# Performance work log

Hardware: AMD Instinct MI355X
Metric: run time of the kernel (lower is better)

## Reference

```python
import jax, jax.numpy as jnp
import numpy as np

K = 20
HID = 64
NUM_CLASSES = 50
BIG = 1e10  # effectively-infinite distance for self-loop exclusion


def knn_idx(x, k):
    # x: [N, d] -> idx: [N, k] indices of k nearest neighbors in feature space (excluding self)
    sq = jnp.sum(x * x, axis=1)
    dist = sq[:, None] + sq[None, :] - 2.0 * (x @ x.T)  # [N, N]
    n = x.shape[0]
    dist = dist.at[jnp.arange(n), jnp.arange(n)].set(BIG)
    _, idx = jax.lax.top_k(-dist, k)
    return idx


def edge_conv(x, k, W, b):
    # DynamicEdgeConv: message = relu(Linear(cat[x_i, x_j - x_i])), aggr = max over k neighbors
    idx = knn_idx(x, k)                      # [N, k]
    xj = x[idx]                              # [N, k, d] neighbor gather
    xi = jnp.broadcast_to(x[:, None, :], xj.shape)
    feat = jnp.concatenate([xi, xj - xi], axis=-1)   # [N, k, 2d]
    h = jax.nn.relu(jnp.einsum('nkf,fo->nko', feat, W) + b)
    return jnp.max(h, axis=1)                # [N, out]


def setup_inputs() -> dict:
    key = jax.random.key(0)
    ks = jax.random.split(key, 16)
    def lin(kw, fan_in, fan_out):
        s = 1.0 / np.sqrt(fan_in)
        return jax.random.uniform(kw, (fan_in, fan_out), jnp.float32, -s, s)
    inp = {
        'x':  jax.random.normal(ks[0], (8192, 3), jnp.float32),
        'W1': lin(ks[1], 2 * 3, HID),      'b1': jnp.zeros((HID,), jnp.float32),
        'W2': lin(ks[2], 2 * HID, HID),    'b2': jnp.zeros((HID,), jnp.float32),
        'W3': lin(ks[3], 2 * HID, HID),    'b3': jnp.zeros((HID,), jnp.float32),
        'Wl': lin(ks[4], 3 * HID, 1024),   'bl': jnp.zeros((1024,), jnp.float32),
        'Wm1': lin(ks[5], 1024, 256),      'bm1': jnp.zeros((256,), jnp.float32),
        'Wm2': lin(ks[6], 256, 128),       'bm2': jnp.zeros((128,), jnp.float32),
        'Wo': lin(ks[7], 128, NUM_CLASSES),'bo': jnp.zeros((NUM_CLASSES,), jnp.float32),
    }
    return inp


def reference(x, W1, b1, W2, b2, W3, b3, Wl, bl, Wm1, bm1, Wm2, bm2, Wo, bo):
    x1 = edge_conv(x, K, W1, b1)     # [N, 64], kNN on raw 3-D points
    x2 = edge_conv(x1, K, W2, b2)    # [N, 64], kNN recomputed in feature space
    x3 = edge_conv(x2, K, W3, b3)    # [N, 64]
    h = jnp.concatenate([x1, x2, x3], axis=1)            # [N, 192]
    h = jax.nn.relu(h @ Wl + bl)                         # lin1: MLP([192, 1024])
    h = jax.nn.relu(h @ Wm1 + bm1)                       # MLP([1024, 256]) (dropout: eval mode)
    h = jax.nn.relu(h @ Wm2 + bm2)                       # MLP([256, 128])
    out = h @ Wo + bo                                    # final Linear
    return jax.nn.log_softmax(out, axis=-1)
```

## Files before the change

### kernel.cpp

```cpp
#include <hip/hip_runtime.h>
#include <math.h>

#define NPTS 8192
#define KNN 20
#define NLISTS 32

#define OFF_SQ   0
#define OFF_IDX  8192
#define OFF_A    172032
#define OFF_B    696320
#define OFF_CAT  1220608
#define OFF_H1   2793472
#define OFF_H2   11182080
#define OFF_H3   13279232
#define OFF_PART OFF_H1
#define OFF_PACK (OFF_H1 + 5242880)
#define PACK_ELEMS 262144
#define OFF_WT   OFF_A

typedef __attribute__((ext_vector_type(8))) short bf16x8;
typedef __attribute__((ext_vector_type(16))) float f32x16;

__device__ inline unsigned umed3(unsigned a, unsigned b, unsigned c) {
    unsigned d;
    asm("v_med3_u32 %0, %1, %2, %3" : "=v"(d) : "v"(a), "v"(b), "v"(c));
    return d;
}

__device__ inline unsigned short f2bf(float f) {
    unsigned u = __float_as_uint(f);
    u += 0x7FFFu + ((u >> 16) & 1u);
    return (unsigned short)(u >> 16);
}

template<int D>
__global__ __launch_bounds__(256)
void sqnorm_kernel(const float* __restrict__ X, int stride, float* __restrict__ sq) {
    int n = blockIdx.x * blockDim.x + threadIdx.x;
    if (n < NPTS) {
        float s = 0.f;
        #pragma unroll
        for (int f = 0; f < D; ++f) {
            float v = X[(size_t)n * stride + f];
            s = fmaf(v, v, s);
        }
        sq[n] = s;
    }
}

template<int D, int KP>
__global__ __launch_bounds__(256)
void prepack_kernel(const float* __restrict__ X, int stride,
                    unsigned short* __restrict__ Xhi, unsigned short* __restrict__ Xlo,
                    unsigned short* __restrict__ Yhi, unsigned short* __restrict__ Ylo) {
    int t2 = blockIdx.x * 256 + threadIdx.x;
    int t = t2 * 2;
    int n = t >> (KP == 64 ? 6 : 4);
    int k = t & (KP - 1);
    float xv[2];
    xv[0] = (k     < D) ? X[(size_t)n * stride + k]     : 0.f;
    xv[1] = (k + 1 < D) ? X[(size_t)n * stride + k + 1] : 0.f;
    ushort2 hx, lx, hy, ly;
    unsigned short* hxp = (unsigned short*)&hx;
    unsigned short* lxp = (unsigned short*)&lx;
    unsigned short* hyp = (unsigned short*)&hy;
    unsigned short* lyp = (unsigned short*)&ly;
    #pragma unroll
    for (int e = 0; e < 2; ++e) {
        float x = xv[e];
        unsigned short hi = f2bf(x);
        float hif = __uint_as_float((unsigned)hi << 16);
        unsigned short lo = f2bf(x - hif);
        float y = -2.f * x;
        unsigned short yhi = f2bf(y);
        float yhif = __uint_as_float((unsigned)yhi << 16);
        unsigned short ylo = f2bf(y - yhif);
        hxp[e] = hi; lxp[e] = lo; hyp[e] = yhi; lyp[e] = ylo;
    }
    *(ushort2*)&Xhi[t] = hx;
    *(ushort2*)&Xlo[t] = lx;
    *(ushort2*)&Yhi[t] = hy;
    *(ushort2*)&Ylo[t] = ly;
}

template<int K, int NBITS>
__global__ __launch_bounds__(256)
void prepack_w(const float* __restrict__ W,
               unsigned short* __restrict__ Thi, unsigned short* __restrict__ Tlo) {
    const int N = 1 << NBITS;
    int t = blockIdx.x * 256 + threadIdx.x;
    int k = t >> NBITS, n = t & (N - 1);
    float x = W[t];
    unsigned short hi = f2bf(x);
    float hif = __uint_as_float((unsigned)hi << 16);
    unsigned short lo = f2bf(x - hif);
    Thi[(size_t)n * K + k] = hi;
    Tlo[(size_t)n * K + k] = lo;
}

template<int KP>
__global__ __launch_bounds__(256, 4)
void knnA_mfma(const unsigned short* __restrict__ Yhi, const unsigned short* __restrict__ Ylo,
               const unsigned short* __restrict__ Xhi, const unsigned short* __restrict__ Xlo,
               const float* __restrict__ sq, unsigned int* __restrict__ part) {
    constexpr int NS = KP / 16;
    constexpr int NT = 8;
    const int wave = threadIdx.x >> 6, lane = threadIdx.x & 63;
    const int col = lane & 31;
    const int h   = lane >> 5;
    const int bi  = (blockIdx.x * 4 + wave) * 32 + col;
    const int jbase = blockIdx.y * 256;

    bf16x8 bhi[NS], blo[NS];
    #pragma unroll
    for (int s = 0; s < NS; ++s) {
        bhi[s] = *(const bf16x8*)&Xhi[(size_t)bi * KP + s * 16 + h * 8];
        blo[s] = *(const bf16x8*)&Xlo[(size_t)bi * KP + s * 16 + h * 8];
    }
    const float sqi = sq[bi];

    unsigned top[KNN];
    #pragma unroll
    for (int k = 0; k < KNN; ++k) top[k] = 0xFFFFFFFFu;

    for (int jt = 0; jt < NT; ++jt) {
        const int j0 = jbase + jt * 32;
        const int aj = j0 + col;
        f32x16 C;
        #pragma unroll
        for (int q = 0; q < 4; ++q) {
            const float4 s4 = *(const float4*)&sq[j0 + h * 4 + q * 8];
            C[q * 4 + 0] = sqi + s4.x;
            C[q * 4 + 1] = sqi + s4.y;
            C[q * 4 + 2] = sqi + s4.z;
            C[q * 4 + 3] = sqi + s4.w;
        }
        #pragma unroll
        for (int s = 0; s < NS; ++s) {
            bf16x8 ahi = *(const bf16x8*)&Yhi[(size_t)aj * KP + s * 16 + h * 8];
            bf16x8 alo = *(const bf16x8*)&Ylo[(size_t)aj * KP + s * 16 + h * 8];
            C = __builtin_amdgcn_mfma_f32_32x32x16_bf16(ahi, bhi[s], C, 0, 0, 0);
            C = __builtin_amdgcn_mfma_f32_32x32x16_bf16(ahi, blo[s], C, 0, 0, 0);
            C = __builtin_amdgcn_mfma_f32_32x32x16_bf16(alo, bhi[s], C, 0, 0, 0);
        }
        #pragma unroll
        for (int q = 0; q < 4; ++q) {
            const int jq = j0 + h * 4 + q * 8;
            #pragma unroll
            for (int t = 0; t < 4; ++t) {
                const int j = jq + t;
                float d = fmaxf(C[q * 4 + t], 0.f);
                unsigned key = (__float_as_uint(d) & 0xFFFFE000u) | (unsigned)j;
                if (j == bi) key = 0xFFFFFFFFu;
                #pragma unroll
                for (int p = KNN - 1; p >= 1; --p)
                    top[p] = umed3(key, top[p - 1], top[p]);
                top[0] = min(top[0], key);
            }
        }
    }

    {
        bool done = false;
        #pragma unroll
        for (int k = 0; k < KNN; ++k) {
            unsigned c = __shfl_xor(top[k], 32);
            if (!done) done = __all(c >= top[KNN - 1]);
            if (!done) {
                #pragma unroll
                for (int p = KNN - 1; p >= 1; --p)
                    top[p] = umed3(c, top[p - 1], top[p]);
                top[0] = min(top[0], c);
            }
        }
    }

    if (h == 0) {
        unsigned* o = part + ((size_t)bi * NLISTS + blockIdx.y) * KNN;
        #pragma unroll
        for (int k = 0; k < KNN; ++k) o[k] = top[k];
    }
}

__global__ __launch_bounds__(256)
void knnB_kernel(const unsigned int* __restrict__ part, int* __restrict__ idx_out) {
    const int wave = threadIdx.x >> 6, lane = threadIdx.x & 63;
    const int half = lane >> 5;
    const int l = lane & 31;
    const int row = (blockIdx.x * 4 + wave) * 2 + half;

    unsigned top[KNN];
    const unsigned* p = part + ((size_t)row * NLISTS + l) * KNN;
    #pragma unroll
    for (int k = 0; k < KNN; k += 4) {
        uint4 v = *(const uint4*)(p + k);
        top[k] = v.x; top[k + 1] = v.y; top[k + 2] = v.z; top[k + 3] = v.w;
    }

    #pragma unroll
    for (int mi = 0; mi < 5; ++mi) {
        const int m = 1 << mi;
        bool done = false;
        #pragma unroll
        for (int k = 0; k < KNN; ++k) {
            unsigned c = __shfl_xor(top[k], m);
            if (!done) done = __all(c >= top[KNN - 1]);
            if (!done) {
                #pragma unroll
                for (int q = KNN - 1; q >= 1; --q)
                    top[q] = umed3(c, top[q - 1], top[q]);
                top[0] = min(top[0], c);
            }
        }
    }

    if (l == 0) {
        #pragma unroll
        for (int k = 0; k < KNN; ++k)
            idx_out[(size_t)row * KNN + k] = (int)(top[k] & 0x1FFFu);
    }
}

template<int D>
__global__ __launch_bounds__(256)
void featAB_kernel(const float* __restrict__ X, int stride, const float* __restrict__ W,
                   float* __restrict__ A, float* __restrict__ B) {
    const int wave = threadIdx.x >> 6, lane = threadIdx.x & 63;
    const int n = blockIdx.x * 4 + wave;
    float a = 0.f, b = 0.f;
    const float* xp = X + (size_t)n * stride;
    #pragma unroll
    for (int f = 0; f < D; ++f) {
        float xf = xp[f];
        a = fmaf(xf, W[(size_t)f * 64 + lane], a);
        b = fmaf(xf, W[(size_t)(D + f) * 64 + lane], b);
    }
    A[(size_t)n * 64 + lane] = a;
    B[(size_t)n * 64 + lane] = b;
}

__global__ __launch_bounds__(256)
void edge_fuse_kernel(const float* __restrict__ A, const float* __restrict__ B,
                      const int* __restrict__ idx, const float* __restrict__ bias,
                      float* __restrict__ out, int ostride,
                      float* __restrict__ sqo,
                      unsigned short* __restrict__ Xhi, unsigned short* __restrict__ Xlo,
                      unsigned short* __restrict__ Yhi, unsigned short* __restrict__ Ylo) {
    const int wave = threadIdx.x >> 6, lane = threadIdx.x & 63;
    const int n = blockIdx.x * 4 + wave;
    const float base = A[(size_t)n * 64 + lane] - B[(size_t)n * 64 + lane] + bias[lane];
    float m = -INFINITY;
    #pragma unroll 4
    for (int k = 0; k < KNN; ++k) {
        int j = idx[(size_t)n * KNN + k];
        m = fmaxf(m, base + B[(size_t)j * 64 + lane]);
    }
    m = fmaxf(m, 0.f);
    out[(size_t)n * ostride + lane] = m;

    float s = m * m;
    #pragma unroll
    for (int off = 32; off; off >>= 1) s += __shfl_xor(s, off);
    if (lane == 0) sqo[n] = s;

    unsigned short hi = f2bf(m);
    float hif = __uint_as_float((unsigned)hi << 16);
    unsigned short lo = f2bf(m - hif);
    float y = -2.f * m;
    unsigned short yhi = f2bf(y);
    float yhif = __uint_as_float((unsigned)yhi << 16);
    unsigned short ylo = f2bf(y - yhif);
    Xhi[(size_t)n * 64 + lane] = hi;
    Xlo[(size_t)n * 64 + lane] = lo;
    Yhi[(size_t)n * 64 + lane] = yhi;
    Ylo[(size_t)n * 64 + lane] = ylo;
}

__global__ __launch_bounds__(256)
void edge_agg_kernel(const float* __restrict__ A, const float* __restrict__ B,
                     const int* __restrict__ idx, const float* __restrict__ bias,
                     float* __restrict__ out, int ostride) {
    const int wave = threadIdx.x >> 6, lane = threadIdx.x & 63;
    const int n = blockIdx.x * 4 + wave;
    const float base = A[(size_t)n * 64 + lane] - B[(size_t)n * 64 + lane] + bias[lane];
    float m = -INFINITY;
    #pragma unroll 4
    for (int k = 0; k < KNN; ++k) {
        int j = idx[(size_t)n * KNN + k];
        m = fmaxf(m, base + B[(size_t)j * 64 + lane]);
    }
    out[(size_t)n * ostride + lane] = fmaxf(m, 0.f);
}

template<int K, int N, int CTW>
__global__ __launch_bounds__(256, 3)
void gemm_mfma_relu(const float* __restrict__ A,
                    const unsigned short* __restrict__ Whi, const unsigned short* __restrict__ Wlo,
                    const float* __restrict__ bias, float* __restrict__ C) {
    const int wave = threadIdx.x >> 6, lane = threadIdx.x & 63;
    const int col = lane & 31, h = lane >> 5;
    const int r0 = blockIdx.x * 32;
    const int nb = blockIdx.y * (CTW * 128) + wave * (CTW * 32);
    const float* arow = A + (size_t)(r0 + col) * K + h * 8;

    f32x16 acc[CTW];
    #pragma unroll
    for (int c = 0; c < CTW; ++c)
        #pragma unroll
        for (int r = 0; r < 16; ++r) acc[c][r] = 0.f;

    #pragma unroll 4
    for (int s = 0; s < K / 16; ++s) {
        float4 f0 = *(const float4*)(arow + s * 16);
        float4 f1 = *(const float4*)(arow + s * 16 + 4);
        bf16x8 ahi, alo;
        {
            float xv[8] = {f0.x, f0.y, f0.z, f0.w, f1.x, f1.y, f1.z, f1.w};
            #pragma unroll
            for (int e = 0; e < 8; ++e) {
                unsigned u = __float_as_uint(xv[e]);
                ahi[e] = (short)(u >> 16);
                float d = xv[e] - __uint_as_float(u & 0xFFFF0000u);
                alo[e] = (short)(__float_as_uint(d) >> 16);
            }
        }
        #pragma unroll
        for (int c = 0; c < CTW; ++c) {
            const size_t wb = (size_t)(nb + c * 32 + col) * K + s * 16 + h * 8;
            bf16x8 bhi = *(const bf16x8*)&Whi[wb];
            bf16x8 blo = *(const bf16x8*)&Wlo[wb];
            acc[c] = __builtin_amdgcn_mfma_f32_32x32x16_bf16(ahi, bhi, acc[c], 0, 0, 0);
            acc[c] = __builtin_amdgcn_mfma_f32_32x32x16_bf16(alo, bhi, acc[c], 0, 0, 0);
            acc[c] = __builtin_amdgcn_mfma_f32_32x32x16_bf16(ahi, blo, acc[c], 0, 0, 0);
        }
    }

    #pragma unroll
    for (int c = 0; c < CTW; ++c) {
        const int n = nb + c * 32 + col;
        const float b = bias[n];
        #pragma unroll
        for (int q = 0; q < 4; ++q)
            #pragma unroll
            for (int t = 0; t < 4; ++t) {
                const int rl = 4 * h + 8 * q + t;
                C[(size_t)(r0 + rl) * N + n] = fmaxf(acc[c][q * 4 + t] + b, 0.f);
            }
    }
}

__global__ __launch_bounds__(256)
void final_kernel(const float* __restrict__ H, const float* __restrict__ Wo,
                  const float* __restrict__ bo, float* __restrict__ out) {
    const int wave = threadIdx.x >> 6, lane = threadIdx.x & 63;
    const int n = blockIdx.x * 4 + wave;
    float v = -INFINITY;
    if (lane < 50) {
        float a = bo[lane];
        const float* h = H + (size_t)n * 128;
        #pragma unroll 4
        for (int f = 0; f < 128; ++f) a = fmaf(h[f], Wo[f * 50 + lane], a);
        v = a;
    }
    float mx = v;
    #pragma unroll
    for (int off = 32; off; off >>= 1) mx = fmaxf(mx, __shfl_xor(mx, off));
    float e = (lane < 50) ? expf(v - mx) : 0.f;
    float s = e;
    #pragma unroll
    for (int off = 32; off; off >>= 1) s += __shfl_xor(s, off);
    if (lane < 50) out[(size_t)n * 50 + lane] = v - mx - logf(s);
}

extern "C" void kernel_launch(void* const* d_in, const int* in_sizes, int n_in,
                              void* d_out, int out_size, void* d_ws, size_t ws_size,
                              hipStream_t stream) {
    const float* x   = (const float*)d_in[0];
    const float* W1  = (const float*)d_in[1];
    const float* b1  = (const float*)d_in[2];
    const float* W2  = (const float*)d_in[3];
    const float* b2  = (const float*)d_in[4];
    const float* W3  = (const float*)d_in[5];
    const float* b3  = (const float*)d_in[6];
    const float* Wl  = (const float*)d_in[7];
    const float* bl  = (const float*)d_in[8];
    const float* Wm1 = (const float*)d_in[9];
    const float* bm1 = (const float*)d_in[10];
    const float* Wm2 = (const float*)d_in[11];
    const float* bm2 = (const float*)d_in[12];
    const float* Wo  = (const float*)d_in[13];
    const float* bo  = (const float*)d_in[14];

    float* ws   = (float*)d_ws;
    float* sq   = ws + OFF_SQ;
    int*   idx  = (int*)(ws + OFF_IDX);
    float* Abuf = ws + OFF_A;
    float* Bbuf = ws + OFF_B;
    float* cat  = ws + OFF_CAT;
    float* h1   = ws + OFF_H1;
    unsigned int* part = (unsigned int*)(ws + OFF_PART);
    unsigned short* Phi = (unsigned short*)(ws + OFF_PACK);
    unsigned short* Plo = (unsigned short*)(ws + OFF_PACK + PACK_ELEMS);
    unsigned short* Qhi = (unsigned short*)(ws + OFF_PACK + 2 * PACK_ELEMS);
    unsigned short* Qlo = (unsigned short*)(ws + OFF_PACK + 3 * PACK_ELEMS);
    float* h2   = ws + OFF_H2;
    float* h3   = ws + OFF_H3;
    unsigned short* WlT_hi  = (unsigned short*)(ws + OFF_WT);
    unsigned short* WlT_lo  = (unsigned short*)(ws + OFF_WT + 98304);
    unsigned short* Wm1T_hi = (unsigned short*)(ws + OFF_WT + 196608);
    unsigned short* Wm1T_lo = (unsigned short*)(ws + OFF_WT + 327680);
    unsigned short* Wm2T_hi = (unsigned short*)(ws + OFF_WT + 458752);
    unsigned short* Wm2T_lo = (unsigned short*)(ws + OFF_WT + 475136);
    float* out  = (float*)d_out;

    dim3 b256(256);
    dim3 gknn(64, 32);

    sqnorm_kernel<3><<<32, b256, 0, stream>>>(x, 3, sq);
    prepack_kernel<3, 16><<<256, b256, 0, stream>>>(x, 3, Phi, Plo, Qhi, Qlo);
    knnA_mfma<16><<<gknn, b256, 0, stream>>>(Qhi, Qlo, Phi, Plo, sq, part);
    knnB_kernel<<<1024, b256, 0, stream>>>(part, idx);
    featAB_kernel<3><<<2048, b256, 0, stream>>>(x, 3, W1, Abuf, Bbuf);
    edge_fuse_kernel<<<2048, b256, 0, stream>>>(Abuf, Bbuf, idx, b1, cat + 0, 192,
                                                sq, Phi, Plo, Qhi, Qlo);

    knnA_mfma<64><<<gknn, b256, 0, stream>>>(Qhi, Qlo, Phi, Plo, sq, part);
    knnB_kernel<<<1024, b256, 0, stream>>>(part, idx);
    featAB_kernel<64><<<2048, b256, 0, stream>>>(cat + 0, 192, W2, Abuf, Bbuf);
    edge_fuse_kernel<<<2048, b256, 0, stream>>>(Abuf, Bbuf, idx, b2, cat + 64, 192,
                                                sq, Phi, Plo, Qhi, Qlo);

    knnA_mfma<64><<<gknn, b256, 0, stream>>>(Qhi, Qlo, Phi, Plo, sq, part);
    knnB_kernel<<<1024, b256, 0, stream>>>(part, idx);
    featAB_kernel<64><<<2048, b256, 0, stream>>>(cat + 64, 192, W3, Abuf, Bbuf);
    edge_agg_kernel<<<2048, b256, 0, stream>>>(Abuf, Bbuf, idx, b3, cat + 128, 192);

    prepack_w<192, 10><<<768, b256, 0, stream>>>(Wl, WlT_hi, WlT_lo);
    prepack_w<1024, 8><<<1024, b256, 0, stream>>>(Wm1, Wm1T_hi, Wm1T_lo);
    prepack_w<256, 7><<<128, b256, 0, stream>>>(Wm2, Wm2T_hi, Wm2T_lo);

    dim3 g1(256, 4);
    gemm_mfma_relu<192, 1024, 2><<<g1, b256, 0, stream>>>(cat, WlT_hi, WlT_lo, bl, h1);
    dim3 g2(256, 1);
    gemm_mfma_relu<1024, 256, 2><<<g2, b256, 0, stream>>>(h1, Wm1T_hi, Wm1T_lo, bm1, h2);
    dim3 g3(256, 1);
    gemm_mfma_relu<256, 128, 1><<<g3, b256, 0, stream>>>(h2, Wm2T_hi, Wm2T_lo, bm2, h3);
    final_kernel<<<2048, b256, 0, stream>>>(h3, Wo, bo, out);
}
```

Measured before the change: 523.0 us.

## Software-pipeline kNN MFMA tiles with double-buffered accumulators and prefetched operands

Restructures the kNN distance loop in knnA_mfma to process two 32-column tiles per iteration with two accumulators, so the top-k insertion of one tile can overlap the MFMA chain of the next. Operand fragments for the next tiles are loaded ahead of use. The launch bound drops from 4 to 2 blocks per SM to give room for the extra registers. Lower occupancy may reduce latency hiding elsewhere.

```diff
diff --git a/kernel.cpp b/kernel.cpp
--- a/kernel.cpp
+++ b/kernel.cpp
@@ -98,8 +98,26 @@
     Tlo[(size_t)n * K + k] = lo;
 }
 
+#define PROCESS(Cv, j0base)                                                    \
+    do {                                                                       \
+        _Pragma("unroll")                                                      \
+        for (int q = 0; q < 4; ++q) {                                          \
+            _Pragma("unroll")                                                  \
+            for (int t = 0; t < 4; ++t) {                                      \
+                const int j = (j0base) + h * 4 + q * 8 + t;                    \
+                float dd = fmaxf((Cv)[q * 4 + t], 0.f);                        \
+                unsigned key = (__float_as_uint(dd) & 0xFFFFE000u) | (unsigned)j; \
+                if (j == bi) key = 0xFFFFFFFFu;                                \
+                _Pragma("unroll")                                              \
+                for (int p = KNN - 1; p >= 1; --p)                             \
+                    top[p] = umed3(key, top[p - 1], top[p]);                   \
+                top[0] = min(top[0], key);                                     \
+            }                                                                  \
+        }                                                                      \
+    } while (0)
+
 template<int KP>
-__global__ __launch_bounds__(256, 4)
+__global__ __launch_bounds__(256, 2)
 void knnA_mfma(const unsigned short* __restrict__ Yhi, const unsigned short* __restrict__ Ylo,
                const unsigned short* __restrict__ Xhi, const unsigned short* __restrict__ Xlo,
                const float* __restrict__ sq, unsigned int* __restrict__ part) {
@@ -123,42 +141,72 @@
     #pragma unroll
     for (int k = 0; k < KNN; ++k) top[k] = 0xFFFFFFFFu;
 
-    for (int jt = 0; jt < NT; ++jt) {
-        const int j0 = jbase + jt * 32;
+    bf16x8 fA[NS], fB[NS], lo[NS];
+    f32x16 CCa, CCb;
+
+    {
+        const size_t a0 = (size_t)(jbase + col) * KP + h * 8;
+        #pragma unroll
+        for (int s = 0; s < NS; ++s)
+            fA[s] = *(const bf16x8*)&Yhi[a0 + s * 16];
+    }
+
+    #pragma unroll 1
+    for (int jt2 = 0; jt2 < NT; jt2 += 2) {
+        const int j0 = jbase + jt2 * 32;
         const int aj = j0 + col;
-        f32x16 C;
-        #pragma unroll
-        for (int q = 0; q < 4; ++q) {
-            const float4 s4 = *(const float4*)&sq[j0 + h * 4 + q * 8];
-            C[q * 4 + 0] = sqi + s4.x;
-            C[q * 4 + 1] = sqi + s4.y;
-            C[q * 4 + 2] = sqi + s4.z;
-            C[q * 4 + 3] = sqi + s4.w;
-        }
+
+        #pragma unroll
+        for (int s = 0; s < NS; ++s)
+            fB[s] = *(const bf16x8*)&Yhi[(size_t)(aj + 32) * KP + s * 16 + h * 8];
+        #pragma unroll
+        for (int s = 0; s < NS; ++s)
+            lo[s] = *(const bf16x8*)&Ylo[(size_t)aj * KP + s * 16 + h * 8];
+        float4 e0 = *(const float4*)&sq[j0 + h * 4];
+        float4 e1 = *(const float4*)&sq[j0 + h * 4 + 8];
+        float4 e2 = *(const float4*)&sq[j0 + h * 4 + 16];
+        float4 e3 = *(const float4*)&sq[j0 + h * 4 + 24];
+
+        if (jt2 > 0) PROCESS(CCb, j0 - 32);
+
+        CCa[0] = sqi + e0.x; CCa[1] = sqi + e0.y; CCa[2]  = sqi + e0.z; CCa[3]  = sqi + e0.w;
+        CCa[4] = sqi + e1.x; CCa[5] = sqi + e1.y; CCa[6]  = sqi + e1.z; CCa[7]  = sqi + e1.w;
+        CCa[8] = sqi + e2.x; CCa[9] = sqi + e2.y; CCa[10] = sqi + e2.z; CCa[11] = sqi + e2.w;
+        CCa[12] = sqi + e3.x; CCa[13] = sqi + e3.y; CCa[14] = sqi + e3.z; CCa[15] = sqi + e3.w;
         #pragma unroll
         for (int s = 0; s < NS; ++s) {
-            bf16x8 ahi = *(const bf16x8*)&Yhi[(size_t)aj * KP + s * 16 + h * 8];
-            bf16x8 alo = *(const bf16x8*)&Ylo[(size_t)aj * KP + s * 16 + h * 8];
-            C = __builtin_amdgcn_mfma_f32_32x32x16_bf16(ahi, bhi[s], C, 0, 0, 0);
-            C = __builtin_amdgcn_mfma_f32_32x32x16_bf16(ahi, blo[s], C, 0, 0, 0);
-            C = __builtin_amdgcn_mfma_f32_32x32x16_bf16(alo, bhi[s], C, 0, 0, 0);
-        }
-        #pragma unroll
-        for (int q = 0; q < 4; ++q) {
-            const int jq = j0 + h * 4 + q * 8;
+            CCa = __builtin_amdgcn_mfma_f32_32x32x16_bf16(fA[s], bhi[s], CCa, 0, 0, 0);
+            CCa = __builtin_amdgcn_mfma_f32_32x32x16_bf16(fA[s], blo[s], CCa, 0, 0, 0);
+            CCa = __builtin_amdgcn_mfma_f32_32x32x16_bf16(lo[s], bhi[s], CCa, 0, 0, 0);
+        }
+
+        if (jt2 + 2 < NT) {
             #pragma unroll
-            for (int t = 0; t < 4; ++t) {
-                const int j = jq + t;
-                float d = fmaxf(C[q * 4 + t], 0.f);
-                unsigned key = (__float_as_uint(d) & 0xFFFFE000u) | (unsigned)j;
-                if (j == bi) key = 0xFFFFFFFFu;
-                #pragma unroll
-                for (int p = KNN - 1; p >= 1; --p)
-                    top[p] = umed3(key, top[p - 1], top[p]);
-                top[0] = min(top[0], key);
-            }
-        }
-    }
+            for (int s = 0; s < NS; ++s)
+                fA[s] = *(const bf16x8*)&Yhi[(size_t)(aj + 64) * KP + s * 16 + h * 8];
+        }
+        #pragma unroll
+        for (int s = 0; s < NS; ++s)
+            lo[s] = *(const bf16x8*)&Ylo[(size_t)(aj + 32) * KP + s * 16 + h * 8];
+        float4 o0 = *(const float4*)&sq[j0 + 32 + h * 4];
+        float4 o1 = *(const float4*)&sq[j0 + 32 + h * 4 + 8];
+        float4 o2 = *(const float4*)&sq[j0 + 32 + h * 4 + 16];
+        float4 o3 = *(const float4*)&sq[j0 + 32 + h * 4 + 24];
+
+        PROCESS(CCa, j0);
+
+        CCb[0] = sqi + o0.x; CCb[1] = sqi + o0.y; CCb[2]  = sqi + o0.z; CCb[3]  = sqi + o0.w;
+        CCb[4] = sqi + o1.x; CCb[5] = sqi + o1.y; CCb[6]  = sqi + o1.z; CCb[7]  = sqi + o1.w;
+        CCb[8] = sqi + o2.x; CCb[9] = sqi + o2.y; CCb[10] = sqi + o2.z; CCb[11] = sqi + o2.w;
+        CCb[12] = sqi + o3.x; CCb[13] = sqi + o3.y; CCb[14] = sqi + o3.z; CCb[15] = sqi + o3.w;
+        #pragma unroll
+        for (int s = 0; s < NS; ++s) {
+            CCb = __builtin_amdgcn_mfma_f32_32x32x16_bf16(fB[s], bhi[s], CCb, 0, 0, 0);
+            CCb = __builtin_amdgcn_mfma_f32_32x32x16_bf16(fB[s], blo[s], CCb, 0, 0, 0);
+            CCb = __builtin_amdgcn_mfma_f32_32x32x16_bf16(lo[s], bhi[s], CCb, 0, 0, 0);
+        }
+    }
+    PROCESS(CCb, jbase + (NT - 1) * 32);
 
     {
         bool done = false;
```

New measurement: 519.1 us. No clear change (-0.8%).
